# Optimization experiments

Measured on AMD Instinct MI355X. Metric: run time of the kernel, lower is better.

## Reference

```python
import jax, jax.numpy as jnp
from jax import lax
import numpy as np

B_SZ, L, D_MODEL, N_STATE, K_CONV, D_RANK = 2, 1024, 768, 16, 4, 48
DT_MIN, DT_MAX = 1e-4, 0.1


def setup_inputs() -> dict:
    key = jax.random.key(0)
    ks = jax.random.split(key, 8)
    s = 0.02
    x = jax.random.normal(ks[0], (B_SZ, L, D_MODEL), jnp.float32)
    W_in = jax.random.normal(ks[1], (D_MODEL, 2 * D_MODEL), jnp.float32) * s
    conv_w = jax.random.normal(ks[2], (D_MODEL, 1, K_CONV), jnp.float32) * 0.2
    conv_b = jnp.zeros((D_MODEL,), jnp.float32)
    W_x = jax.random.normal(ks[3], (D_MODEL, D_RANK + 2 * N_STATE), jnp.float32) * s
    W_delta = jax.random.normal(ks[4], (D_RANK, D_MODEL), jnp.float32) * s
    b_delta = jnp.zeros((D_MODEL,), jnp.float32)
    # Mamba S4D-real init: A_log = log(1..N) repeated over D
    A_log = jnp.log(jnp.tile(jnp.arange(1, N_STATE + 1, dtype=jnp.float32)[None, :], (D_MODEL, 1)))
    D_param = jnp.ones((D_MODEL,), jnp.float32)
    W_out = jax.random.normal(ks[5], (D_MODEL, D_MODEL), jnp.float32) * s
    return dict(x=x, W_in=W_in, conv_w=conv_w, conv_b=conv_b, W_x=W_x,
                W_delta=W_delta, b_delta=b_delta, A_log=A_log, D_param=D_param, W_out=W_out)


def _selective_scan(u, delta, A, Bm, Cm, Dp):
    # u, delta: (B,L,D); A: (D,N); Bm,Cm: (B,L,N); Dp: (D,)
    dA = jnp.einsum('bld,dn->bldn', delta, A)            # (B,L,D,N)
    dB_u = jnp.einsum('bld,bld,bln->bldn', delta, u, Bm)  # (B,L,D,N)
    # tf.pad(dA[:,1:],[[0,0],[1,1],...])[:,1:] == shift left by one, zero at end
    shifted = jnp.concatenate([dA[:, 1:], jnp.zeros_like(dA[:, :1])], axis=1)
    cs = jnp.flip(jnp.cumsum(jnp.flip(shifted, axis=1), axis=1), axis=1)
    dA_cs = jnp.exp(cs)
    xs = jnp.cumsum(dB_u * dA_cs, axis=1) / (dA_cs + 1e-12)
    y = jnp.einsum('bldn,bln->bld', xs, Cm)
    return y + u * Dp


def reference(x, W_in, conv_w, conv_b, W_x, W_delta, b_delta, A_log, D_param, W_out):
    Bb, Ll, Dm = x.shape
    Kk = conv_w.shape[-1]
    xr = x @ W_in                                   # (B,L,2D)
    xs, res = jnp.split(xr, 2, axis=-1)
    # depthwise causal conv over L (channels_first, groups=D)
    xc = jnp.transpose(xs, (0, 2, 1))               # (B,D,L)
    xc = lax.conv_general_dilated(xc, conv_w, window_strides=(1,),
                                  padding=[(Kk - 1, 0)],
                                  dimension_numbers=('NCL', 'OIL', 'NCL'),
                                  feature_group_count=Dm)
    xc = xc + conv_b[None, :, None]
    xs = jax.nn.silu(jnp.transpose(xc, (0, 2, 1)))  # (B,L,D)
    # SSM parameterization
    A = -jnp.exp(A_log)                             # (D,N)
    xp = xs @ W_x                                   # (B,L,dr+2N)
    dr = W_delta.shape[0]
    Nn = A_log.shape[1]
    delta, Bm, Cm = jnp.split(xp, [dr, dr + Nn], axis=-1)
    delta = jax.nn.softplus(delta @ W_delta + b_delta)
    delta = jnp.clip(delta, DT_MIN, DT_MAX)
    y = _selective_scan(xs, delta, A, Bm, Cm, D_param)
    y = y * jax.nn.silu(res)
    return y @ W_out
```

## Files before the change

### kernel.cpp

```cpp
#include <hip/hip_runtime.h>
#include <math.h>

#define LSEQ 1024
#define DM   768
#define NS   16
#define DR   48
#define BSZ  2
#define R2   (BSZ*LSEQ)
#define NC   64
#define LC   (LSEQ/NC)
#define KSP  6
#define XPR  (R2*80)

typedef __bf16 bf16x2 __attribute__((ext_vector_type(2)));
typedef __bf16 bf16x4 __attribute__((ext_vector_type(4)));
typedef __bf16 bf16x8 __attribute__((ext_vector_type(8)));
typedef float  f32x4  __attribute__((ext_vector_type(4)));

template<int ABF16, int OUTBF16, int EPI, int ASUM>
__global__ __launch_bounds__(256) void gemm_t64(const void* __restrict__ Av,
                                                const float* __restrict__ B,
                                                void* __restrict__ Cv,
                                                void* __restrict__ C1v,
                                                const float* __restrict__ bias,
                                                int K, int Ksrc, int lda, int ldb, int ldc,
                                                int split) {
    __shared__ __align__(16) __bf16 As[64][40];
    __shared__ __align__(16) __bf16 Bs[64][40];
    const int tid  = threadIdx.x;
    const int lane = tid & 63;
    const int wave = tid >> 6;
    const int r = lane & 15, q = lane >> 4;
    const int n0 = blockIdx.x * 64, m0 = blockIdx.y * 64;

    const int arow = tid >> 2, ak8 = (tid & 3) * 8;
    const int nq = tid & 15, kg = (tid >> 4) & 7;

    f32x4 zero = {0.f, 0.f, 0.f, 0.f};
    f32x4 acc[4];
    #pragma unroll
    for (int nt = 0; nt < 4; ++nt) acc[nt] = zero;

    f32x4 a0, a1, b_pf[4];
    bf16x8 a8;
    auto loadA = [&](int kbase) {
        if (ABF16) {
            const __bf16* A = (const __bf16*)Av;
            a8 = *(const bf16x8*)(A + (size_t)(m0 + arow) * lda + kbase + ak8);
        } else if (ASUM > 0) {
            const float* A = (const float*)Av;
            a0 = zero; a1 = zero;
            if (kbase + ak8 < Ksrc) {
                #pragma unroll
                for (int s2 = 0; s2 < ASUM; ++s2) {
                    f32x4 v = *(const f32x4*)(A + (size_t)s2 * XPR
                                              + (size_t)(m0 + arow) * lda + kbase + ak8);
                    a0[0] += v[0]; a0[1] += v[1]; a0[2] += v[2]; a0[3] += v[3];
                }
            }
            if (kbase + ak8 + 4 < Ksrc) {
                #pragma unroll
                for (int s2 = 0; s2 < ASUM; ++s2) {
                    f32x4 v = *(const f32x4*)(A + (size_t)s2 * XPR
                                              + (size_t)(m0 + arow) * lda + kbase + ak8 + 4);
                    a1[0] += v[0]; a1[1] += v[1]; a1[2] += v[2]; a1[3] += v[3];
                }
            }
        } else {
            const float* A = (const float*)Av;
            a0 = (kbase + ak8     < Ksrc)
                 ? *(const f32x4*)(A + (size_t)(m0 + arow) * lda + kbase + ak8)     : zero;
            a1 = (kbase + ak8 + 4 < Ksrc)
                 ? *(const f32x4*)(A + (size_t)(m0 + arow) * lda + kbase + ak8 + 4) : zero;
        }
    };
    auto loadB = [&](int kbase) {
        #pragma unroll
        for (int i = 0; i < 4; ++i) {
            int k = kbase + kg * 4 + i;
            b_pf[i] = (k < Ksrc) ? *(const f32x4*)(B + (size_t)k * ldb + n0 + nq * 4) : zero;
        }
    };

    loadA(0);
    if (tid < 128) loadB(0);

    const int KT = K / 32;
    for (int kt = 0; kt < KT; ++kt) {
        if (ABF16) {
            *(bf16x8*)&As[arow][ak8] = a8;
        } else {
            bf16x4 p0 = {(__bf16)a0[0], (__bf16)a0[1], (__bf16)a0[2], (__bf16)a0[3]};
            bf16x4 p1 = {(__bf16)a1[0], (__bf16)a1[1], (__bf16)a1[2], (__bf16)a1[3]};
            *(bf16x4*)&As[arow][ak8]     = p0;
            *(bf16x4*)&As[arow][ak8 + 4] = p1;
        }
        if (tid < 128) {
            #pragma unroll
            for (int c = 0; c < 4; ++c) {
                bf16x4 pk = {(__bf16)b_pf[0][c], (__bf16)b_pf[1][c],
                             (__bf16)b_pf[2][c], (__bf16)b_pf[3][c]};
                *(bf16x4*)&Bs[nq * 4 + c][kg * 4] = pk;
            }
        }
        __syncthreads();
        if (kt + 1 < KT) {
            loadA((kt + 1) * 32);
            if (tid < 128) loadB((kt + 1) * 32);
        }
        bf16x8 af = *(const bf16x8*)&As[wave * 16 + r][q * 8];
        #pragma unroll
        for (int nt = 0; nt < 4; ++nt) {
            bf16x8 bfr = *(const bf16x8*)&Bs[nt * 16 + r][q * 8];
            acc[nt] = __builtin_amdgcn_mfma_f32_16x16x32_bf16(af, bfr, acc[nt], 0, 0, 0);
        }
        __syncthreads();
    }
    const int rowb = m0 + wave * 16 + q * 4;
    void* Cd = Cv;
    int nbase = n0;
    if (EPI == 1 && n0 >= split) { Cd = C1v; nbase = n0 - split; }
    #pragma unroll
    for (int nt = 0; nt < 4; ++nt) {
        int col = nbase + nt * 16 + r;
        float bcol = (EPI == 2) ? bias[n0 + nt * 16 + r] : 0.f;
        #pragma unroll
        for (int rr = 0; rr < 4; ++rr) {
            float z = acc[nt][rr];
            if (EPI == 2) {
                z += bcol;
                z = (z > 20.f) ? z : log1pf(expf(z));
                z = fminf(fmaxf(z, 1e-4f), 0.1f);
            }
            if (OUTBF16)
                ((__bf16*)Cd)[(size_t)(rowb + rr) * ldc + col] = (__bf16)z;
            else
                ((float*)Cd)[(size_t)(rowb + rr) * ldc + col] = z;
        }
    }
}

__global__ __launch_bounds__(256) void conv_silu_b(const __bf16* __restrict__ xs,
                                                   const float* __restrict__ cw,
                                                   const float* __restrict__ cb,
                                                   __bf16* __restrict__ u) {
    const int idx = blockIdx.x * 256 + threadIdx.x;
    const int r  = idx / (DM / 2);
    const int dh = idx - r * (DM / 2);
    const int d  = dh * 2;
    const int l  = r & (LSEQ - 1);
    f32x4 w0 = *(const f32x4*)(cw + d * 4);
    f32x4 w1 = *(const f32x4*)(cw + d * 4 + 4);
    float a0 = cb[d], a1 = cb[d + 1];
    #pragma unroll
    for (int k = 0; k < 4; ++k) {
        if (l - 3 + k >= 0) {
            bf16x2 v = *(const bf16x2*)(xs + (size_t)(r - 3 + k) * DM + d);
            a0 += (float)v[0] * w0[k];
            a1 += (float)v[1] * w1[k];
        }
    }
    float u0 = a0 / (1.f + expf(-a0));
    float u1 = a1 / (1.f + expf(-a1));
    bf16x2 o = {(__bf16)u0, (__bf16)u1};
    *(bf16x2*)(u + (size_t)r * DM + d) = o;
}

__global__ __launch_bounds__(256) void gemm_wx_sk(const __bf16* __restrict__ U,
                                                  const float* __restrict__ Wx,
                                                  float* __restrict__ xpp) {
    __shared__ __align__(16) __bf16 As2[64][40];
    __shared__ __align__(16) __bf16 Ws[80][40];
    const int tid  = threadIdx.x;
    const int lane = tid & 63;
    const int wave = tid >> 6;
    const int r = lane & 15, q = lane >> 4;
    const int m0 = blockIdx.x * 64;
    const int kbase = blockIdx.y * (768 / KSP);
    const int arow = tid >> 2, ak8 = (tid & 3) * 8;
    const int nq = tid % 20, kq = tid / 20;

    f32x4 acc[5];
    #pragma unroll
    for (int nt = 0; nt < 5; ++nt) acc[nt] = {0.f, 0.f, 0.f, 0.f};

    bf16x8 a_pf;
    f32x4 w_pf[4];
    a_pf = *(const bf16x8*)(U + (size_t)(m0 + arow) * DM + kbase + ak8);
    if (tid < 160) {
        #pragma unroll
        for (int i = 0; i < 4; ++i)
            w_pf[i] = *(const f32x4*)(Wx + (size_t)(kbase + kq * 4 + i) * 80 + nq * 4);
    }

    const int KT = (768 / KSP) / 32;
    for (int kt = 0; kt < KT; ++kt) {
        *(bf16x8*)&As2[arow][ak8] = a_pf;
        if (tid < 160) {
            #pragma unroll
            for (int c = 0; c < 4; ++c) {
                bf16x4 pk = {(__bf16)w_pf[0][c], (__bf16)w_pf[1][c],
                             (__bf16)w_pf[2][c], (__bf16)w_pf[3][c]};
                *(bf16x4*)&Ws[nq * 4 + c][kq * 4] = pk;
            }
        }
        __syncthreads();
        if (kt + 1 < KT) {
            int k0 = kbase + (kt + 1) * 32;
            a_pf = *(const bf16x8*)(U + (size_t)(m0 + arow) * DM + k0 + ak8);
            if (tid < 160) {
                #pragma unroll
                for (int i = 0; i < 4; ++i)
                    w_pf[i] = *(const f32x4*)(Wx + (size_t)(k0 + kq * 4 + i) * 80 + nq * 4);
            }
        }
        bf16x8 af = *(const bf16x8*)&As2[wave * 16 + r][q * 8];
        #pragma unroll
        for (int nt = 0; nt < 5; ++nt) {
            bf16x8 bfr = *(const bf16x8*)&Ws[nt * 16 + r][q * 8];
            acc[nt] = __builtin_amdgcn_mfma_f32_16x16x32_bf16(af, bfr, acc[nt], 0, 0, 0);
        }
        __syncthreads();
    }
    #pragma unroll
    for (int nt = 0; nt < 5; ++nt) {
        int col  = nt * 16 + r;
        int rowb = m0 + wave * 16 + q * 4;
        #pragma unroll
        for (int rr = 0; rr < 4; ++rr)
            xpp[((size_t)blockIdx.y * XPR + (size_t)(rowb + rr) * 80 + col)] = acc[nt][rr];
    }
}

__global__ __launch_bounds__(128) void scan_part1(const __bf16* __restrict__ delta,
                                                  const __bf16* __restrict__ u,
                                                  const float* __restrict__ xpp,
                                                  const float* __restrict__ A_log,
                                                  float* __restrict__ Eprod,
                                                  float* __restrict__ Hend,
                                                  float* __restrict__ SDel) {
    __shared__ float sB[LC][NS];
    const int tid = threadIdx.x;
    const int blk = blockIdx.x;
    const int ch = blk % NC;
    const int dg = (blk / NC) % (DM / 128);
    const int b  = blk / (NC * (DM / 128));
    const int d  = dg * 128 + tid;
    const int l0 = ch * LC;
    const int bd = b * DM + d;

    for (int i = tid; i < LC * NS; i += 128) {
        int l = i >> 4, n = i & 15;
        size_t off = (size_t)(b * LSEQ + l0 + l) * 80 + DR + n;
        float s = 0.f;
        #pragma unroll
        for (int ks = 0; ks < KSP; ++ks) s += xpp[(size_t)ks * XPR + off];
        sB[l][n] = s;
    }
    float c[NS];
    #pragma unroll
    for (int n = 0; n < NS; ++n) c[n] = -__expf(A_log[d * NS + n]);
    __syncthreads();

    float h[NS], ep[NS];
    #pragma unroll
    for (int n = 0; n < NS; ++n) { h[n] = 0.f; ep[n] = 1.f; }
    float pd = 0.f;
    for (int l = 0; l < LC; ++l) {
        size_t rr = (size_t)(b * LSEQ + l0 + l);
        float dlt = (float)delta[rr * DM + d];
        float uu  = (float)u[rr * DM + d];
        pd += dlt;
        float du = dlt * uu;
        #pragma unroll
        for (int n = 0; n < NS; ++n) {
            float e = __expf(c[n] * dlt);
            h[n]  = e * h[n] + du * sB[l][n];
            ep[n] *= e;
        }
    }
    #pragma unroll
    for (int n = 0; n < NS; ++n) {
        size_t idx = ((size_t)ch * NS + n) * (BSZ * DM) + bd;
        Eprod[idx] = ep[n];
        Hend[idx]  = h[n];
    }
    SDel[(size_t)ch * (BSZ * DM) + bd] = pd;
}

__global__ __launch_bounds__(64) void scan_combine(const float* __restrict__ Eprod,
                                                   float* __restrict__ Hend,
                                                   float* __restrict__ SDel,
                                                   float* __restrict__ TD) {
    const int t = blockIdx.x * 64 + threadIdx.x;
    const int BD = BSZ * DM;
    float H = 0.f;
    for (int cg = 0; cg < NC; cg += 8) {
        float e[8], he[8];
        #pragma unroll
        for (int j = 0; j < 8; ++j) {
            size_t idx = (size_t)(cg + j) * (NS * BD) + t;
            e[j]  = Eprod[idx];
            he[j] = Hend[idx];
        }
        #pragma unroll
        for (int j = 0; j < 8; ++j) {
            size_t idx = (size_t)(cg + j) * (NS * BD) + t;
            Hend[idx] = H;
            H = e[j] * H + he[j];
        }
    }
    if (t < BD) {
        float pd = 0.f;
        for (int cg = 0; cg < NC; cg += 8) {
            float s[8];
            #pragma unroll
            for (int j = 0; j < 8; ++j) s[j] = SDel[(size_t)(cg + j) * BD + t];
            #pragma unroll
            for (int j = 0; j < 8; ++j) {
                SDel[(size_t)(cg + j) * BD + t] = pd;
                pd += s[j];
            }
        }
        TD[t] = pd;
    }
}

__global__ __launch_bounds__(128) void scan_part3(const __bf16* __restrict__ delta,
                                                  const __bf16* __restrict__ u,
                                                  const float* __restrict__ xpp,
                                                  const __bf16* __restrict__ res,
                                                  const float* __restrict__ A_log,
                                                  const float* __restrict__ Dp,
                                                  const float* __restrict__ Hin,
                                                  const float* __restrict__ PD0,
                                                  const float* __restrict__ TD,
                                                  __bf16* __restrict__ g) {
    __shared__ float sB[LC][NS];
    __shared__ float sC[LC][NS];
    const int tid = threadIdx.x;
    const int blk = blockIdx.x;
    const int ch = blk % NC;
    const int dg = (blk / NC) % (DM / 128);
    const int b  = blk / (NC * (DM / 128));
    const int d  = dg * 128 + tid;
    const int l0 = ch * LC;
    const int bd = b * DM + d;

    for (int i = tid; i < LC * NS; i += 128) {
        int l = i >> 4, n = i & 15;
        size_t offB = (size_t)(b * LSEQ + l0 + l) * 80 + DR + n;
        float sb = 0.f, sc = 0.f;
        #pragma unroll
        for (int ks = 0; ks < KSP; ++ks) {
            sb += xpp[(size_t)ks * XPR + offB];
            sc += xpp[(size_t)ks * XPR + offB + NS];
        }
        sB[l][n] = sb;
        sC[l][n] = sc;
    }
    float c[NS], h[NS];
    #pragma unroll
    for (int n = 0; n < NS; ++n) {
        c[n] = -__expf(A_log[d * NS + n]);
        h[n] = Hin[((size_t)ch * NS + n) * (BSZ * DM) + bd];
    }
    float pd = PD0[(size_t)ch * (BSZ * DM) + bd];
    const float td = TD[bd];
    const float dp = Dp[d];
    __syncthreads();

    for (int l = 0; l < LC; ++l) {
        size_t rr = (size_t)(b * LSEQ + l0 + l);
        float dlt = (float)delta[rr * DM + d];
        float uu  = (float)u[rr * DM + d];
        float rv  = (float)res[rr * DM + d];
        pd += dlt;
        float du = dlt * uu;
        float x = td - pd;
        float y = 0.f;
        #pragma unroll
        for (int n = 0; n < NS; ++n) {
            float e = __expf(c[n] * dlt);
            h[n] = e * h[n] + du * sB[l][n];
            float P = __expf(-c[n] * x);
            float den = 1.0f + 1e-12f * P;
            y += h[n] * sC[l][n] * __builtin_amdgcn_rcpf(den);
        }
        y += uu * dp;
        float sig = __builtin_amdgcn_rcpf(1.f + __expf(-rv));
        g[rr * DM + d] = (__bf16)(y * rv * sig);
    }
}

extern "C" void kernel_launch(void* const* d_in, const int* in_sizes, int n_in,
                              void* d_out, int out_size, void* d_ws, size_t ws_size,
                              hipStream_t stream) {
    const float* x       = (const float*)d_in[0];
    const float* W_in    = (const float*)d_in[1];
    const float* conv_w  = (const float*)d_in[2];
    const float* conv_b  = (const float*)d_in[3];
    const float* W_x     = (const float*)d_in[4];
    const float* W_delta = (const float*)d_in[5];
    const float* b_delta = (const float*)d_in[6];
    const float* A_log   = (const float*)d_in[7];
    const float* D_param = (const float*)d_in[8];
    const float* W_out   = (const float*)d_in[9];
    float* out = (float*)d_out;

    char* p = (char*)d_ws;
    __bf16* xs    = (__bf16*)p;  p += (size_t)R2 * DM * 2;
    __bf16* res   = (__bf16*)p;  p += (size_t)R2 * DM * 2;
    __bf16* u     = (__bf16*)p;  p += (size_t)R2 * DM * 2;
    __bf16* delta = (__bf16*)p;  p += (size_t)R2 * DM * 2;
    float*  xpp   = (float*)p;   p += (size_t)KSP * XPR * 4;
    float*  Eprod = (float*)p;   p += (size_t)NC * NS * BSZ * DM * 4;
    float*  Hend  = (float*)p;   p += (size_t)NC * NS * BSZ * DM * 4;
    float*  SDel  = (float*)p;   p += (size_t)NC * BSZ * DM * 4;
    float*  TD    = (float*)p;
    __bf16* g     = u;

    gemm_t64<0, 1, 1, 0><<<dim3(1536 / 64, R2 / 64), 256, 0, stream>>>(
        x, W_in, xs, res, nullptr, 768, 768, 768, 1536, 768, 768);
    conv_silu_b<<<(R2 * DM / 2) / 256, 256, 0, stream>>>(xs, conv_w, conv_b, u);
    gemm_wx_sk<<<dim3(R2 / 64, KSP), 256, 0, stream>>>(u, W_x, xpp);
    gemm_t64<0, 1, 2, KSP><<<dim3(DM / 64, R2 / 64), 256, 0, stream>>>(
        xpp, W_delta, delta, delta, b_delta, 64, 48, 80, 768, 768, 1 << 30);
    scan_part1<<<BSZ * (DM / 128) * NC, 128, 0, stream>>>(delta, u, xpp, A_log,
                                                          Eprod, Hend, SDel);
    scan_combine<<<(NS * BSZ * DM) / 64, 64, 0, stream>>>(Eprod, Hend, SDel, TD);
    scan_part3<<<BSZ * (DM / 128) * NC, 128, 0, stream>>>(delta, u, xpp, res, A_log, D_param,
                                                          Hend, SDel, TD, g);
    gemm_t64<1, 0, 0, 0><<<dim3(DM / 64, R2 / 64), 256, 0, stream>>>(
        g, W_out, out, out, nullptr, 768, 768, 768, 768, 768, 1 << 30);
}
```

Measured before the change: 186.5 us.

## Fuse depthwise conv+SiLU into split-K W_x GEMM, staging u in LDS

Merges the causal depthwise conv/SiLU kernel into the split-K W_x projection GEMM. Each block computes u for its 64 rows by 128 channels, writes it both to global memory (needed by the scan) and to shared memory, and loads all four W_x k-slices into LDS up front. The MFMA loop then runs from LDS without per-step syncs. This removes one launch and the global re-read of u, in exchange for more LDS per block and a serial conv phase before any MFMA work.

```diff
diff --git a/kernel.cpp b/kernel.cpp
--- a/kernel.cpp
+++ b/kernel.cpp
@@ -140,87 +140,80 @@
     }
 }
 
-__global__ __launch_bounds__(256) void conv_silu_b(const __bf16* __restrict__ xs,
-                                                   const float* __restrict__ cw,
-                                                   const float* __restrict__ cb,
-                                                   __bf16* __restrict__ u) {
-    const int idx = blockIdx.x * 256 + threadIdx.x;
-    const int r  = idx / (DM / 2);
-    const int dh = idx - r * (DM / 2);
-    const int d  = dh * 2;
-    const int l  = r & (LSEQ - 1);
-    f32x4 w0 = *(const f32x4*)(cw + d * 4);
-    f32x4 w1 = *(const f32x4*)(cw + d * 4 + 4);
-    float a0 = cb[d], a1 = cb[d + 1];
-    #pragma unroll
-    for (int k = 0; k < 4; ++k) {
-        if (l - 3 + k >= 0) {
-            bf16x2 v = *(const bf16x2*)(xs + (size_t)(r - 3 + k) * DM + d);
-            a0 += (float)v[0] * w0[k];
-            a1 += (float)v[1] * w1[k];
-        }
-    }
-    float u0 = a0 / (1.f + expf(-a0));
-    float u1 = a1 / (1.f + expf(-a1));
-    bf16x2 o = {(__bf16)u0, (__bf16)u1};
-    *(bf16x2*)(u + (size_t)r * DM + d) = o;
-}
-
-__global__ __launch_bounds__(256) void gemm_wx_sk(const __bf16* __restrict__ U,
-                                                  const float* __restrict__ Wx,
-                                                  float* __restrict__ xpp) {
-    __shared__ __align__(16) __bf16 As2[64][40];
-    __shared__ __align__(16) __bf16 Ws[80][40];
+__global__ __launch_bounds__(256) void convwx_sk(const __bf16* __restrict__ xs,
+                                                 const float* __restrict__ cw,
+                                                 const float* __restrict__ cb,
+                                                 const float* __restrict__ Wx,
+                                                 __bf16* __restrict__ u,
+                                                 float* __restrict__ xpp) {
+    __shared__ __align__(16) __bf16 uS[4][64 * 40 + 8];
+    __shared__ __align__(16) __bf16 Ws[4][80 * 40 + 8];
     const int tid  = threadIdx.x;
     const int lane = tid & 63;
     const int wave = tid >> 6;
     const int r = lane & 15, q = lane >> 4;
     const int m0 = blockIdx.x * 64;
-    const int kbase = blockIdx.y * (768 / KSP);
-    const int arow = tid >> 2, ak8 = (tid & 3) * 8;
-    const int nq = tid % 20, kq = tid / 20;
+    const int kbase = blockIdx.y * 128;
+
+    if (tid < 160) {
+        const int nq = tid % 20, kq = tid / 20;
+        #pragma unroll
+        for (int s = 0; s < 4; ++s) {
+            f32x4 wp[4];
+            #pragma unroll
+            for (int i = 0; i < 4; ++i)
+                wp[i] = *(const f32x4*)(Wx + (size_t)(kbase + s * 32 + kq * 4 + i) * 80
+                                        + nq * 4);
+            #pragma unroll
+            for (int c2 = 0; c2 < 4; ++c2) {
+                bf16x4 pk = {(__bf16)wp[0][c2], (__bf16)wp[1][c2],
+                             (__bf16)wp[2][c2], (__bf16)wp[3][c2]};
+                *(bf16x4*)&Ws[s][(nq * 4 + c2) * 40 + kq * 4] = pk;
+            }
+        }
+    }
+    {
+        const int dh = tid & 63;
+        const int rg = tid >> 6;
+        const int cl = dh * 2;
+        const int d  = kbase + cl;
+        f32x4 wA = *(const f32x4*)(cw + d * 4);
+        f32x4 wB = *(const f32x4*)(cw + (d + 1) * 4);
+        const float cbA = cb[d], cbB = cb[d + 1];
+        #pragma unroll
+        for (int i = 0; i < 16; ++i) {
+            int row = rg * 16 + i;
+            int rr  = m0 + row;
+            int l   = rr & (LSEQ - 1);
+            float a0 = cbA, a1 = cbB;
+            #pragma unroll
+            for (int k = 0; k < 4; ++k) {
+                if (l - 3 + k >= 0) {
+                    bf16x2 v = *(const bf16x2*)(xs + (size_t)(rr - 3 + k) * DM + d);
+                    a0 += (float)v[0] * wA[k];
+                    a1 += (float)v[1] * wB[k];
+                }
+            }
+            float u0 = a0 / (1.f + expf(-a0));
+            float u1 = a1 / (1.f + expf(-a1));
+            bf16x2 o = {(__bf16)u0, (__bf16)u1};
+            *(bf16x2*)(u + (size_t)rr * DM + d) = o;
+            *(bf16x2*)&uS[cl >> 5][row * 40 + (cl & 31)] = o;
+        }
+    }
+    __syncthreads();
 
     f32x4 acc[5];
     #pragma unroll
     for (int nt = 0; nt < 5; ++nt) acc[nt] = {0.f, 0.f, 0.f, 0.f};
-
-    bf16x8 a_pf;
-    f32x4 w_pf[4];
-    a_pf = *(const bf16x8*)(U + (size_t)(m0 + arow) * DM + kbase + ak8);
-    if (tid < 160) {
-        #pragma unroll
-        for (int i = 0; i < 4; ++i)
-            w_pf[i] = *(const f32x4*)(Wx + (size_t)(kbase + kq * 4 + i) * 80 + nq * 4);
-    }
-
-    const int KT = (768 / KSP) / 32;
-    for (int kt = 0; kt < KT; ++kt) {
-        *(bf16x8*)&As2[arow][ak8] = a_pf;
-        if (tid < 160) {
-            #pragma unroll
-            for (int c = 0; c < 4; ++c) {
-                bf16x4 pk = {(__bf16)w_pf[0][c], (__bf16)w_pf[1][c],
-                             (__bf16)w_pf[2][c], (__bf16)w_pf[3][c]};
-                *(bf16x4*)&Ws[nq * 4 + c][kq * 4] = pk;
-            }
-        }
-        __syncthreads();
-        if (kt + 1 < KT) {
-            int k0 = kbase + (kt + 1) * 32;
-            a_pf = *(const bf16x8*)(U + (size_t)(m0 + arow) * DM + k0 + ak8);
-            if (tid < 160) {
-                #pragma unroll
-                for (int i = 0; i < 4; ++i)
-                    w_pf[i] = *(const f32x4*)(Wx + (size_t)(k0 + kq * 4 + i) * 80 + nq * 4);
-            }
-        }
-        bf16x8 af = *(const bf16x8*)&As2[wave * 16 + r][q * 8];
+    #pragma unroll
+    for (int s = 0; s < 4; ++s) {
+        bf16x8 af = *(const bf16x8*)&uS[s][(wave * 16 + r) * 40 + q * 8];
         #pragma unroll
         for (int nt = 0; nt < 5; ++nt) {
-            bf16x8 bfr = *(const bf16x8*)&Ws[nt * 16 + r][q * 8];
+            bf16x8 bfr = *(const bf16x8*)&Ws[s][(nt * 16 + r) * 40 + q * 8];
             acc[nt] = __builtin_amdgcn_mfma_f32_16x16x32_bf16(af, bfr, acc[nt], 0, 0, 0);
         }
-        __syncthreads();
     }
     #pragma unroll
     for (int nt = 0; nt < 5; ++nt) {
@@ -228,7 +221,7 @@
         int rowb = m0 + wave * 16 + q * 4;
         #pragma unroll
         for (int rr = 0; rr < 4; ++rr)
-            xpp[((size_t)blockIdx.y * XPR + (size_t)(rowb + rr) * 80 + col)] = acc[nt][rr];
+            xpp[(size_t)blockIdx.y * XPR + (size_t)(rowb + rr) * 80 + col] = acc[nt][rr];
     }
 }
 
@@ -422,8 +415,7 @@
 
     gemm_t64<0, 1, 1, 0><<<dim3(1536 / 64, R2 / 64), 256, 0, stream>>>(
         x, W_in, xs, res, nullptr, 768, 768, 768, 1536, 768, 768);
-    conv_silu_b<<<(R2 * DM / 2) / 256, 256, 0, stream>>>(xs, conv_w, conv_b, u);
-    gemm_wx_sk<<<dim3(R2 / 64, KSP), 256, 0, stream>>>(u, W_x, xpp);
+    convwx_sk<<<dim3(R2 / 64, KSP), 256, 0, stream>>>(xs, conv_w, conv_b, W_x, u, xpp);
     gemm_t64<0, 1, 2, KSP><<<dim3(DM / 64, R2 / 64), 256, 0, stream>>>(
         xpp, W_delta, delta, delta, b_delta, 64, 48, 80, 768, 768, 1 << 30);
     scan_part1<<<BSZ * (DM / 128) * NC, 128, 0, stream>>>(delta, u, xpp, A_log,
```

New measurement: 185.4 us. No clear change (-0.6%).
